# Optimization experiments

Hardware: AMD Instinct MI355X
Metric: run time of the kernel (lower is better)

Reference implementation:

```python
import jax, jax.numpy as jnp
import numpy as np

B, NQ, NK, QS, KS, H, VD = 16, 64, 512, 256, 256, 256, 256


def setup_inputs() -> dict:
    key = jax.random.key(0)
    k1, k2, k3, k4, k5, k6, k7 = jax.random.split(key, 7)
    return {
        "queries": jax.random.normal(k1, (B, NQ, QS), dtype=jnp.float32),
        "keys": jax.random.normal(k2, (B, NK, KS), dtype=jnp.float32),
        "values": jax.random.normal(k3, (B, NK, VD), dtype=jnp.float32),
        "valid_lens": jax.random.randint(k4, (B,), 1, NK + 1, dtype=jnp.int32),
        # learned params (nn.Linear with bias=False): W_q [QS,H], W_k [KS,H], w_v [H]
        "W_q": jax.random.normal(k5, (QS, H), dtype=jnp.float32) / np.sqrt(QS),
        "W_k": jax.random.normal(k6, (KS, H), dtype=jnp.float32) / np.sqrt(KS),
        "w_v": jax.random.normal(k7, (H,), dtype=jnp.float32) / np.sqrt(H),
    }


def reference(queries, keys, values, valid_lens, W_q, W_k, w_v):
    # project: q [B,nq,H], k [B,nk,H]
    q = jnp.einsum("bqd,dh->bqh", queries, W_q)
    k = jnp.einsum("bkd,dh->bkh", keys, W_k)
    # broadcast-add -> tanh -> score reduction via w_v: [B,nq,nk]
    features = jnp.tanh(q[:, :, None, :] + k[:, None, :, :])  # [B,nq,nk,H]
    scores = jnp.einsum("bqkh,h->bqk", features, w_v)
    # masked softmax over keys (positions >= valid_len masked out)
    mask = jnp.arange(scores.shape[-1])[None, None, :] < valid_lens[:, None, None]
    scores = jnp.where(mask, scores, -1e6)
    attn = jax.nn.softmax(scores, axis=-1)
    # weighted sum of values (dropout p=0 / eval mode => identity)
    return jnp.einsum("bqk,bkv->bqv", attn, values)
```

## Files before the change

kernel.cpp:

```cpp
#include <hip/hip_runtime.h>
#include <hip/hip_bf16.h>

#define BB 16
#define NQ 64
#define NK 512
#define HD 256

typedef __attribute__((ext_vector_type(8))) short short8;
typedef __attribute__((ext_vector_type(4))) float f32x4;

__device__ __forceinline__ ushort bf16_rne(float v) {
    unsigned u = __float_as_uint(v);
    return (ushort)((u + 0x7FFFu + ((u >> 16) & 1u)) >> 16);
}
__device__ __forceinline__ float bf16_to_f(ushort h) {
    return __uint_as_float(((unsigned)h) << 16);
}

__global__ __launch_bounds__(256, 2) void proj_fused2(
    const float* __restrict__ queries, const float* __restrict__ keys,
    const float* __restrict__ W_q, const float* __restrict__ W_k,
    float* __restrict__ qp, float* __restrict__ kp, float scale)
{
    __shared__ ushort AsH[64 * 64], AsL[64 * 64];
    __shared__ ushort BsH[64 * 64], BsL[64 * 64];

    const float* A; const float* W; float* C; int rows0;
    const int bx = blockIdx.x;
    if (bx < 16) { A = queries; W = W_q; C = qp; rows0 = bx * 64; }
    else         { A = keys;    W = W_k; C = kp; rows0 = (bx - 16) * 64; }
    const int cols0 = blockIdx.y * 64;

    const int t = threadIdx.x, lane = t & 63, wave = t >> 6;
    const int quad = lane >> 4, l15 = lane & 15;
    const int sr  = t >> 2;
    const int sc2 = (t & 3) * 2;

    f32x4 acc[4];
    #pragma unroll
    for (int j = 0; j < 4; ++j) acc[j] = (f32x4){0.f, 0.f, 0.f, 0.f};

    for (int k0 = 0; k0 < 256; k0 += 64) {
        const float* arow = &A[(size_t)(rows0 + sr) * 256 + k0 + sc2 * 8];
        float4 a0 = *(const float4*)&arow[0];
        float4 a1 = *(const float4*)&arow[4];
        float4 a2 = *(const float4*)&arow[8];
        float4 a3 = *(const float4*)&arow[12];
        float wvv[16];
        {
            const float* wsrc = &W[(size_t)(k0 + sc2 * 8) * 256 + cols0 + sr];
            #pragma unroll
            for (int e = 0; e < 16; ++e)
                wvv[e] = wsrc[(size_t)e * 256];
        }

        __syncthreads();

        float av[16] = {a0.x, a0.y, a0.z, a0.w, a1.x, a1.y, a1.z, a1.w,
                        a2.x, a2.y, a2.z, a2.w, a3.x, a3.y, a3.z, a3.w};
        short8 ah0, ah1, al0, al1, bh0, bh1, bl0, bl1;
        #pragma unroll
        for (int e = 0; e < 8; ++e) {
            ushort h0 = bf16_rne(av[e]);
            ushort h1 = bf16_rne(av[8 + e]);
            ah0[e] = (short)h0;
            ah1[e] = (short)h1;
            al0[e] = (short)bf16_rne(av[e] - bf16_to_f(h0));
            al1[e] = (short)bf16_rne(av[8 + e] - bf16_to_f(h1));
            ushort w0 = bf16_rne(wvv[e]);
            ushort w1 = bf16_rne(wvv[8 + e]);
            bh0[e] = (short)w0;
            bh1[e] = (short)w1;
            bl0[e] = (short)bf16_rne(wvv[e] - bf16_to_f(w0));
            bl1[e] = (short)bf16_rne(wvv[8 + e] - bf16_to_f(w1));
        }
        {
            int s0 = sr * 8 + ((sc2 + 0) ^ (sr & 7));
            int s1 = sr * 8 + ((sc2 + 1) ^ (sr & 7));
            *(short8*)&AsH[s0 * 8] = ah0;
            *(short8*)&AsH[s1 * 8] = ah1;
            *(short8*)&AsL[s0 * 8] = al0;
            *(short8*)&AsL[s1 * 8] = al1;
            *(short8*)&BsH[s0 * 8] = bh0;
            *(short8*)&BsH[s1 * 8] = bh1;
            *(short8*)&BsL[s0 * 8] = bl0;
            *(short8*)&BsL[s1 * 8] = bl1;
        }
        __syncthreads();

        #pragma unroll
        for (int ks = 0; ks < 2; ++ks) {
            const int c = ks * 4 + quad;
            short8 aH, aL, bH[4], bL[4];
            {
                int r = wave * 16 + l15;
                int slot = r * 8 + (c ^ (r & 7));
                aH = *(const short8*)&AsH[slot * 8];
                aL = *(const short8*)&AsL[slot * 8];
            }
            #pragma unroll
            for (int ns = 0; ns < 4; ++ns) {
                int n = ns * 16 + l15;
                int slot = n * 8 + (c ^ (n & 7));
                bH[ns] = *(const short8*)&BsH[slot * 8];
                bL[ns] = *(const short8*)&BsL[slot * 8];
            }
            #pragma unroll
            for (int ns = 0; ns < 4; ++ns)
                acc[ns] = __builtin_amdgcn_mfma_f32_16x16x32_bf16(aH, bH[ns], acc[ns], 0, 0, 0);
            #pragma unroll
            for (int ns = 0; ns < 4; ++ns)
                acc[ns] = __builtin_amdgcn_mfma_f32_16x16x32_bf16(aL, bH[ns], acc[ns], 0, 0, 0);
            #pragma unroll
            for (int ns = 0; ns < 4; ++ns)
                acc[ns] = __builtin_amdgcn_mfma_f32_16x16x32_bf16(aH, bL[ns], acc[ns], 0, 0, 0);
        }
    }

    const int rbase = rows0 + wave * 16 + quad * 4;
    #pragma unroll
    for (int ns = 0; ns < 4; ++ns) {
        int col = cols0 + ns * 16 + l15;
        #pragma unroll
        for (int r = 0; r < 4; ++r)
            C[(size_t)(rbase + r) * 256 + col] =
                __builtin_amdgcn_exp2f(acc[ns][r] * scale);
    }
}

__global__ __launch_bounds__(512, 4) void score_pv_seg5(
    const float* __restrict__ qp,
    const float* __restrict__ kp,
    const float* __restrict__ values,
    const int*   __restrict__ vlens,
    const float* __restrict__ w_v,
    float* __restrict__ pO,
    float* __restrict__ pL)
{
    __shared__ float eq[8][260];
    __shared__ float wv[HD];
    __shared__ float Ps[8][66];
    __shared__ float sP[8][66];
    __shared__ float part[4][8][260];

    const int b   = blockIdx.x & 15;
    const int qt  = blockIdx.x >> 4;
    const int seg = blockIdx.y;
    const int vl  = vlens[b];
    if (seg * 64 >= vl) return;

    const int t = threadIdx.x, lane = t & 63, wave = t >> 6;
    const int kq = wave & 3;
    const int hh = wave >> 2;
    const int key = kq * 16 + (lane >> 2);
    const int ch  = lane & 3;
    const int kg  = seg * 64 + key;

    const float* krow = kp + ((size_t)b * NK + kg) * HD + hh * 128 + ch * 4;
    float4 ek[8];
    #pragma unroll
    for (int j = 0; j < 8; ++j) ek[j] = *(const float4*)&krow[j * 16];

    const float* qsrc = qp + ((size_t)b * NQ + qt * 8) * HD;
    {
        int row = t >> 6, c4 = (t & 63) * 4;
        *(float4*)&eq[row][c4] = *(const float4*)&qsrc[(size_t)row * HD + c4];
    }
    if (t < 64) *(float4*)&wv[t * 4] = *(const float4*)&w_v[t * 4];
    __syncthreads();

    float Wsum;
    {
        float ws = wv[lane] + wv[lane + 64] + wv[lane + 128] + wv[lane + 192];
        #pragma unroll
        for (int off = 32; off; off >>= 1) ws += __shfl_xor(ws, off);
        Wsum = ws;
    }

    float s[8] = {0.f, 0.f, 0.f, 0.f, 0.f, 0.f, 0.f, 0.f};
    #pragma unroll
    for (int j = 0; j < 8; ++j) {
        const int h = hh * 128 + j * 16 + ch * 4;
        float4 e4 = ek[j];
        float4 w4 = *(const float4*)&wv[h];
        #pragma unroll
        for (int qi = 0; qi < 8; ++qi) {
            float4 q4 = *(const float4*)&eq[qi][h];
            float p0 = fmaf(q4.x, e4.x, 1.f);
            float p1 = fmaf(q4.y, e4.y, 1.f);
            float p2 = fmaf(q4.z, e4.z, 1.f);
            float p3 = fmaf(q4.w, e4.w, 1.f);
            float d01 = p0 * p1;
            float d23 = p2 * p3;
            float n01 = fmaf(w4.x, p1, w4.y * p0);
            float n23 = fmaf(w4.z, p3, w4.w * p2);
            float num = fmaf(d01, n23, d23 * n01);
            float r   = __builtin_amdgcn_rcpf(d01 * d23);
            s[qi] = fmaf(num, r, s[qi]);
        }
    }
    #pragma unroll
    for (int qi = 0; qi < 8; ++qi) {
        s[qi] += __shfl_xor(s[qi], 1);
        s[qi] += __shfl_xor(s[qi], 2);
    }
    if (hh == 1 && ch == 0) {
        #pragma unroll
        for (int qi = 0; qi < 8; ++qi) sP[qi][key] = s[qi];
    }
    __syncthreads();
    const float L2E = 1.4426950408889634f;
    if (hh == 0 && ch == 0) {
        const bool masked = (kg >= vl);
        #pragma unroll
        for (int qi = 0; qi < 8; ++qi) {
            float sv = fmaf(-2.f, s[qi] + sP[qi][key], Wsum);
            Ps[qi][key] = masked ? 0.f : __builtin_amdgcn_exp2f(sv * L2E);
        }
    }
    __syncthreads();

    const float* vbase = values + ((size_t)b * NK + seg * 64 + kq * 16) * HD;
    float4 vv[4];
    #pragma unroll
    for (int i = 0; i < 4; ++i)
        vv[i] = *(const float4*)&vbase[(size_t)i * HD + lane * 4];

    {
        float l = Ps[wave][lane];
        #pragma unroll
        for (int off = 32; off; off >>= 1) l += __shfl_xor(l, off);
        if (lane == 0)
            pL[(((size_t)(b * 8 + qt) * 8 + seg)) * 8 + wave] = l;
    }

    f32x4 acc[4];
    #pragma unroll
    for (int r = 0; r < 4; ++r) acc[r] = (f32x4){0.f, 0.f, 0.f, 0.f};
    #pragma unroll
    for (int i = 0; i < 16; ++i) {
        float4 v = vv[i & 3];
        if (i + 4 < 16)
            vv[i & 3] = *(const float4*)&vbase[(size_t)(i + 4) * HD + lane * 4];
        #pragma unroll
        for (int r = 0; r < 4; ++r) {
            float p = Ps[hh * 4 + r][kq * 16 + i];
            acc[r][0] = fmaf(p, v.x, acc[r][0]);
            acc[r][1] = fmaf(p, v.y, acc[r][1]);
            acc[r][2] = fmaf(p, v.z, acc[r][2]);
            acc[r][3] = fmaf(p, v.w, acc[r][3]);
        }
    }
    #pragma unroll
    for (int r = 0; r < 4; ++r)
        *(f32x4*)&part[kq][hh * 4 + r][lane * 4] = acc[r];
    __syncthreads();

    const size_t ob = (((size_t)(b * 8 + qt) * 8 + seg)) * 8 * 256;
    {
        int qi = t >> 6, c4 = (t & 63) * 4;
        float4 p0 = *(const float4*)&part[0][qi][c4];
        float4 p1 = *(const float4*)&part[1][qi][c4];
        float4 p2 = *(const float4*)&part[2][qi][c4];
        float4 p3 = *(const float4*)&part[3][qi][c4];
        float4 o;
        o.x = (p0.x + p1.x) + (p2.x + p3.x);
        o.y = (p0.y + p1.y) + (p2.y + p3.y);
        o.z = (p0.z + p1.z) + (p2.z + p3.z);
        o.w = (p0.w + p1.w) + (p2.w + p3.w);
        *(float4*)&pO[ob + (size_t)qi * 256 + c4] = o;
    }
}

__global__ __launch_bounds__(256) void combine_seg3(
    const float* __restrict__ pO, const float* __restrict__ pL,
    const int* __restrict__ vlens, float* __restrict__ out)
{
    const int b  = blockIdx.x >> 6;
    const int q  = blockIdx.x & 63;
    const int t  = threadIdx.x;
    const int nc = (vlens[b] + 63) >> 6;
    const int qt = q >> 3, qi = q & 7;

    const size_t base = (size_t)(b * 8 + qt) * 8;

    float L = 0.f, acc = 0.f;
    #pragma unroll
    for (int i = 0; i < 8; ++i) {
        if (i < nc) {
            L   += pL[(base + i) * 8 + qi];
            acc += pO[((base + i) * 8 + qi) * 256 + t];
        }
    }
    out[((size_t)(b * 64 + q)) * 256 + t] = acc * __builtin_amdgcn_rcpf(L);
}

extern "C" void kernel_launch(void* const* d_in, const int* in_sizes, int n_in,
                              void* d_out, int out_size, void* d_ws, size_t ws_size,
                              hipStream_t stream) {
    const float* queries = (const float*)d_in[0];
    const float* keys    = (const float*)d_in[1];
    const float* values  = (const float*)d_in[2];
    const int*   vlens   = (const int*)d_in[3];
    const float* W_q     = (const float*)d_in[4];
    const float* W_k     = (const float*)d_in[5];
    const float* w_v     = (const float*)d_in[6];
    float* out = (float*)d_out;

    float* kp = (float*)d_ws;
    float* qp = kp + (size_t)BB * NK * HD;
    float* pO = qp + (size_t)BB * NQ * HD;
    float* pL = pO + (size_t)BB * 8 * 8 * 8 * 256;

    const float SC = 2.885390081777927f;

    proj_fused2<<<dim3(144, 4), 256, 0, stream>>>(queries, keys, W_q, W_k,
                                                  qp, kp, SC);
    score_pv_seg5<<<dim3(128, 8), 512, 0, stream>>>(qp, kp, values, vlens, w_v,
                                                    pO, pL);
    combine_seg3<<<dim3(BB * NQ), 256, 0, stream>>>(pO, pL, vlens, out);
}
```

Before: 111.8 us.

## Fuse split-key combine into score kernel via last-block atomic counter

Removes the separate combine kernel launch. Each score block now increments a per-(batch,query-tile) atomic counter after writing its partials, and the last segment block to arrive reduces the partial outputs and normalisers and writes the final result. The counters are zeroed by the projection kernel. This saves one launch and its gap, at the cost of threadfences, an atomic per block, and a serial tail reduction done by a single block per tile.

```diff
diff --git a/kernel.cpp b/kernel.cpp
--- a/kernel.cpp
+++ b/kernel.cpp
@@ -20,10 +20,14 @@
 __global__ __launch_bounds__(256, 2) void proj_fused2(
     const float* __restrict__ queries, const float* __restrict__ keys,
     const float* __restrict__ W_q, const float* __restrict__ W_k,
-    float* __restrict__ qp, float* __restrict__ kp, float scale)
+    float* __restrict__ qp, float* __restrict__ kp, float scale,
+    int* __restrict__ cnt)
 {
     __shared__ ushort AsH[64 * 64], AsL[64 * 64];
     __shared__ ushort BsH[64 * 64], BsL[64 * 64];
+
+    if (blockIdx.x == 0 && blockIdx.y == 0 && threadIdx.x < 128)
+        cnt[threadIdx.x] = 0;
 
     const float* A; const float* W; float* C; int rows0;
     const int bx = blockIdx.x;
@@ -128,26 +132,30 @@
     }
 }
 
-__global__ __launch_bounds__(512, 4) void score_pv_seg5(
+__global__ __launch_bounds__(512, 4) void score_pv_seg6(
     const float* __restrict__ qp,
     const float* __restrict__ kp,
     const float* __restrict__ values,
     const int*   __restrict__ vlens,
     const float* __restrict__ w_v,
     float* __restrict__ pO,
-    float* __restrict__ pL)
+    float* __restrict__ pL,
+    int*   __restrict__ cnt,
+    float* __restrict__ out)
 {
     __shared__ float eq[8][260];
     __shared__ float wv[HD];
     __shared__ float Ps[8][66];
     __shared__ float sP[8][66];
     __shared__ float part[4][8][260];
+    __shared__ int lastFlag;
 
     const int b   = blockIdx.x & 15;
     const int qt  = blockIdx.x >> 4;
     const int seg = blockIdx.y;
     const int vl  = vlens[b];
     if (seg * 64 >= vl) return;
+    const int nc  = (vl + 63) >> 6;
 
     const int t = threadIdx.x, lane = t & 63, wave = t >> 6;
     const int kq = wave & 3;
@@ -270,29 +278,29 @@
         o.w = (p0.w + p1.w) + (p2.w + p3.w);
         *(float4*)&pO[ob + (size_t)qi * 256 + c4] = o;
     }
-}
-
-__global__ __launch_bounds__(256) void combine_seg3(
-    const float* __restrict__ pO, const float* __restrict__ pL,
-    const int* __restrict__ vlens, float* __restrict__ out)
-{
-    const int b  = blockIdx.x >> 6;
-    const int q  = blockIdx.x & 63;
-    const int t  = threadIdx.x;
-    const int nc = (vlens[b] + 63) >> 6;
-    const int qt = q >> 3, qi = q & 7;
-
-    const size_t base = (size_t)(b * 8 + qt) * 8;
-
-    float L = 0.f, acc = 0.f;
-    #pragma unroll
-    for (int i = 0; i < 8; ++i) {
-        if (i < nc) {
-            L   += pL[(base + i) * 8 + qi];
-            acc += pO[((base + i) * 8 + qi) * 256 + t];
-        }
-    }
-    out[((size_t)(b * 64 + q)) * 256 + t] = acc * __builtin_amdgcn_rcpf(L);
+
+    __threadfence();
+    __syncthreads();
+    if (t == 0)
+        lastFlag = (atomicAdd(&cnt[b * 8 + qt], 1) == nc - 1);
+    __syncthreads();
+    if (lastFlag) {
+        __threadfence();
+        const size_t base = (size_t)(b * 8 + qt) * 8;
+        #pragma unroll
+        for (int it = 0; it < 4; ++it) {
+            int oidx = it * 512 + t;
+            int qrow = oidx >> 8;
+            int vd   = oidx & 255;
+            float L = 0.f, a = 0.f;
+            for (int i = 0; i < nc; ++i) {
+                L += pL[(base + i) * 8 + qrow];
+                a += pO[((base + i) * 8 + qrow) * 256 + vd];
+            }
+            out[((size_t)(b * 64 + qt * 8 + qrow)) * 256 + vd] =
+                a * __builtin_amdgcn_rcpf(L);
+        }
+    }
 }
 
 extern "C" void kernel_launch(void* const* d_in, const int* in_sizes, int n_in,
@@ -311,12 +319,12 @@
     float* qp = kp + (size_t)BB * NK * HD;
     float* pO = qp + (size_t)BB * NQ * HD;
     float* pL = pO + (size_t)BB * 8 * 8 * 8 * 256;
+    int*   cnt = (int*)(pL + (size_t)BB * 8 * 8 * 8);
 
     const float SC = 2.885390081777927f;
 
     proj_fused2<<<dim3(144, 4), 256, 0, stream>>>(queries, keys, W_q, W_k,
-                                                  qp, kp, SC);
-    score_pv_seg5<<<dim3(128, 8), 512, 0, stream>>>(qp, kp, values, vlens, w_v,
-                                                    pO, pL);
-    combine_seg3<<<dim3(BB * NQ), 256, 0, stream>>>(pO, pL, vlens, out);
-}
+                                                  qp, kp, SC, cnt);
+    score_pv_seg6<<<dim3(128, 8), 512, 0, stream>>>(qp, kp, values, vlens, w_v,
+                                                    pO, pL, cnt, out);
+}
```

Measured after the change: 230.0 us. +105.7%, slower.
